# Kernel optimization log

Hardware: AMD Instinct MI355X
Metric: run time of the kernel (lower is better)

The kernel has to match this reference:

```python
import jax, jax.numpy as jnp
import numpy as np

B, S, D_MODEL = 2, 2048, 768
N_QK, D_QK = 16, 16
N_OV, D_OV = 256, 1
VKV = 16
ROT_DIM, ROT_BASE = 16, 10000.0
SCALE = D_QK ** 0.5  # attn_scale defaults to sqrt(d_qk_head)


def _rotary_sin_cos(n_ctx, rotary_dim, base):
    # TransformerLens-style, non-adjacent pairs (GPT-NeoX)
    pos = jnp.arange(n_ctx, dtype=jnp.float32)
    dim = jnp.arange(rotary_dim // 2, dtype=jnp.float32)
    freq = base ** (dim / (rotary_dim / 2))
    freq = jnp.concatenate([freq, freq])  # 'd -> (2 d)'
    angles = pos[:, None] / freq[None, :]  # [n_ctx, rotary_dim]
    return jnp.sin(angles), jnp.cos(angles)


def _apply_rotary(x, sin, cos):
    # x: [B, S, H, d_head]; rotate first ROT_DIM dims, pass through the rest
    s = x.shape[1]
    xr = x[..., :ROT_DIM]
    half = ROT_DIM // 2
    rot = jnp.concatenate([-xr[..., half:], xr[..., :half]], axis=-1)  # rotate_every_two (non-adjacent)
    xr = xr * cos[:s, None, :] + rot * sin[:s, None, :]
    return jnp.concatenate([xr, x[..., ROT_DIM:]], axis=-1) if x.shape[-1] > ROT_DIM else xr


def setup_inputs() -> dict:
    key = jax.random.key(0)
    ks = jax.random.split(key, 6)
    std_qk = np.sqrt(2.0 / (D_MODEL * D_QK))   # kaiming fan_in for [H, d_model, d_head]
    std_v = np.sqrt(2.0 / (D_MODEL * D_OV))
    std_o = np.sqrt(2.0 / (D_OV * D_MODEL))
    std_vk = np.sqrt(2.0 / (N_QK * D_QK))
    return {
        "resid": jax.random.normal(ks[0], (B, S, D_MODEL), jnp.float32),
        "W_Q": jax.random.normal(ks[1], (N_QK, D_MODEL, D_QK), jnp.float32) * std_qk,
        "W_K": jax.random.normal(ks[2], (N_QK, D_MODEL, D_QK), jnp.float32) * std_qk,
        "W_V": jax.random.normal(ks[3], (N_OV, D_MODEL, D_OV), jnp.float32) * std_v,
        "W_O": jax.random.normal(ks[4], (N_OV, D_OV, D_MODEL), jnp.float32) * std_o,
        "b_Q": jnp.zeros((N_QK, D_QK), jnp.float32),
        "b_K": jnp.zeros((N_QK, D_QK), jnp.float32),
        "b_V": jnp.zeros((N_OV, D_OV), jnp.float32),
        "b_O": jnp.zeros((D_MODEL,), jnp.float32),
        "virtual_k": jax.random.normal(ks[5], (VKV, N_QK, D_QK), jnp.float32) * std_vk,
        "virtual_v": jnp.zeros((VKV, N_OV, D_OV), jnp.float32),
    }


def reference(resid, W_Q, W_K, W_V, W_O, b_Q, b_K, b_V, b_O, virtual_k, virtual_v):
    b, s, _ = resid.shape
    sin, cos = _rotary_sin_cos(s, ROT_DIM, ROT_BASE)

    q = jnp.einsum('bsd,hde->bshe', resid, W_Q) + b_Q  # [B,S,N_QK,D_QK]
    k = jnp.einsum('bsd,hde->bshe', resid, W_K) + b_K
    v = jnp.einsum('bsd,hde->bshe', resid, W_V) + b_V  # [B,S,N_OV,1]

    q = _apply_rotary(q, sin, cos)
    k = _apply_rotary(k, sin, cos)

    # append virtual KV along key axis
    k = jnp.concatenate([k, jnp.broadcast_to(virtual_k[None], (b, VKV, N_QK, D_QK))], axis=1)
    v = jnp.concatenate([v, jnp.broadcast_to(virtual_v[None], (b, VKV, N_OV, D_OV))], axis=1)

    scores = jnp.einsum('bqhe,bkhe->bhqk', q, k) / SCALE  # [B,H,S,S+VKV]
    i = jnp.arange(s)[:, None]
    j = jnp.arange(s + VKV)[None, :]
    mask = (j - i) <= VKV  # tril(.., diagonal=VKV)
    scores = jnp.where(mask, scores, -jnp.inf)
    pattern = jax.nn.softmax(scores, axis=-1)
    pattern = jnp.where(jnp.isnan(pattern), 0.0, pattern)

    r = N_OV // N_QK
    v_r = v.transpose(0, 2, 1, 3).reshape(b, N_QK, r, s + VKV, D_OV)  # [B,n_qk,r,K,1]
    z = jnp.einsum('bnqk,bnrkh->bnrqh', pattern, v_r)  # [B,n_qk,r,S,1]
    z = z.reshape(b, N_OV, s, D_OV).transpose(0, 2, 1, 3)  # [B,S,N_OV,1]

    out = jnp.einsum('bqhd,hdm->bqm', z, W_O) + b_O  # [B,S,D_MODEL]
    return out
```

## Files before the change

kernel.cpp:

```cpp
#include <hip/hip_runtime.h>
#include <hip/hip_bf16.h>
#include <math.h>

#define B_   2
#define S_   2048
#define DM   768
#define H_   16
#define C_   256
#define VKV_ 16
#define SK   2064
#define SKP  2080
#define NT_  65

#define TSPLIT 16
#define MAXSP  5
#define NACT   164

typedef __attribute__((ext_vector_type(8))) short short8;
typedef __attribute__((ext_vector_type(4))) short short4v;
typedef __attribute__((ext_vector_type(4))) float f32x4;
typedef __attribute__((ext_vector_type(16))) float f32x16;
typedef __attribute__((ext_vector_type(4))) unsigned uint4v;

#define QSCALE 0.360673760222240851f
#define L2B8   1.6609640474436811f

__device__ __forceinline__ short tobf(float f) {
    union { float f; unsigned u; } x; x.f = f;
    unsigned r = x.u + 0x7FFFu + ((x.u >> 16) & 1u);
    return (short)(r >> 16);
}
__device__ __forceinline__ float frombf_lo(unsigned u) {
    union { unsigned u; float f; } x; x.u = u << 16; return x.f;
}
__device__ __forceinline__ float frombf_hi(unsigned u) {
    union { unsigned u; float f; } x; x.u = u & 0xFFFF0000u; return x.f;
}

__device__ __forceinline__ void gload_lds16(const short* g, short* l) {
    __builtin_amdgcn_global_load_lds(
        (const __attribute__((address_space(1))) unsigned int*)g,
        (__attribute__((address_space(3))) unsigned int*)l, 16, 0, 0);
}

#define NRES (4096*768/4)
#define NWQ  (768*768)
#define NWO  (768*256)
__global__ __launch_bounds__(256) void conv_all(
    const float* __restrict__ resid,
    const float* __restrict__ WQ, const float* __restrict__ WK,
    const float* __restrict__ WV, const float* __restrict__ WO,
    const float* __restrict__ bQ, const float* __restrict__ bK,
    const float* __restrict__ bV,
    const float* __restrict__ vKp, const float* __restrict__ vVp,
    short* __restrict__ Ab, short* __restrict__ Wqkv_t,
    short* __restrict__ WtO, float* __restrict__ bqkv,
    short* __restrict__ Kb2, short* __restrict__ Vt3)
{
    int t = blockIdx.x * 256 + threadIdx.x;
    if (t < NRES) {
        float4 v = *(const float4*)(resid + (size_t)t * 4);
        short4v o = { tobf(v.x), tobf(v.y), tobf(v.z), tobf(v.w) };
        *(short4v*)(Ab + (size_t)t * 4) = o;
        return;
    }
    t -= NRES;
    if (t < NWQ) {
        int cc = t / 768, d = t % 768;
        float w;
        if (cc < 256)      w = WQ[((size_t)(cc >> 4) * DM + d) * 16 + (cc & 15)];
        else if (cc < 512) w = WK[((size_t)((cc - 256) >> 4) * DM + d) * 16 + (cc & 15)];
        else               w = WV[(size_t)(cc - 512) * DM + d];
        Wqkv_t[t] = tobf(w);
        return;
    }
    t -= NWQ;
    if (t < NWO) {
        int c = t & 255, m = t >> 8;
        WtO[t] = tobf(WO[(size_t)c * DM + m]);
        return;
    }
    t -= NWO;
    if (t < 768) {
        bqkv[t] = (t < 256) ? bQ[t] : (t < 512 ? bK[t - 256] : bV[t - 512]);
        return;
    }
    t -= 768;
    if (t < 32 * 32) {
        const int bh = t >> 5;
        const int s  = S_ + (t & 31);
        const int h  = bh & 15;
        short kb[16], vb[16];
        if (s < SK) {
            const int tt = s - S_;
#pragma unroll
            for (int e = 0; e < 16; ++e) {
                kb[e] = tobf(vKp[(size_t)tt * 256 + h * 16 + e]);
                vb[e] = tobf(vVp[(size_t)tt * 256 + h * 16 + e]);
            }
        } else {
#pragma unroll
            for (int e = 0; e < 16; ++e) { kb[e] = 0; vb[e] = 0; }
        }
        const int t5 = s >> 5;
        short* kbase = Kb2 + ((size_t)bh * NT_ + t5) * 512 + (s & 31) * 8;
#pragma unroll
        for (int e = 0; e < 8; ++e)  { kbase[e] = kb[e]; kbase[256 + e] = kb[e + 8]; }
        short* vbase = Vt3 + ((size_t)bh * NT_ + t5) * 1024
                     + ((s >> 4) & 1) * 512 + ((s >> 3) & 1) * 8 + (s & 7);
#pragma unroll
        for (int dv = 0; dv < 16; ++dv) vbase[dv * 16] = vb[dv];
    }
}

__global__ __launch_bounds__(256) void mm_qkv(
    const short* __restrict__ A, const short* __restrict__ Bt,
    const float* __restrict__ bias,
    short* __restrict__ Qb2, short* __restrict__ Kb2, short* __restrict__ Vt3)
{
    __shared__ short As[128 * 64];
    __shared__ short Bs[64 * 64];

    const int tid  = threadIdx.x;
    const int w    = tid >> 6;
    const int lane = tid & 63;
    const int wm   = w >> 1, wn = w & 1;
    const int g    = lane >> 4, c = lane & 15;
    const int m0   = blockIdx.y * 128;
    const int n0   = blockIdx.x * 64;

    f32x4 acc[4][2];
#pragma unroll
    for (int i = 0; i < 4; ++i)
#pragma unroll
        for (int j = 0; j < 2; ++j) acc[i][j] = (f32x4){0.f, 0.f, 0.f, 0.f};

    const int lr = lane >> 3;
    const int lc = lane & 7;

    for (int k0 = 0; k0 < 768; k0 += 64) {
#pragma unroll
        for (int i = 0; i < 4; ++i) {
            const int ch  = i * 4 + w;
            const int row = ch * 8 + lr;
            const int scc = lc ^ (row & 7);
            gload_lds16(A + (size_t)(m0 + row) * 768 + k0 + scc * 8, As + ch * 512);
        }
#pragma unroll
        for (int i = 0; i < 2; ++i) {
            const int ch  = i * 4 + w;
            const int row = ch * 8 + lr;
            const int scc = lc ^ (row & 7);
            gload_lds16(Bt + (size_t)(n0 + row) * 768 + k0 + scc * 8, Bs + ch * 512);
        }
        __syncthreads();
#pragma unroll
        for (int kk = 0; kk < 64; kk += 32) {
            short8 af[4], bf[2];
#pragma unroll
            for (int i = 0; i < 4; ++i) {
                const int row = wm * 64 + i * 16 + c;
                const int sc  = ((kk >> 3) + g) ^ (row & 7);
                af[i] = *(const short8*)(As + row * 64 + sc * 8);
            }
#pragma unroll
            for (int j = 0; j < 2; ++j) {
                const int row = wn * 32 + j * 16 + c;
                const int sc  = ((kk >> 3) + g) ^ (row & 7);
                bf[j] = *(const short8*)(Bs + row * 64 + sc * 8);
            }
#pragma unroll
            for (int i = 0; i < 4; ++i)
#pragma unroll
                for (int j = 0; j < 2; ++j)
                    acc[i][j] = __builtin_amdgcn_mfma_f32_16x16x32_bf16(
                        af[i], bf[j], acc[i][j], 0, 0, 0);
        }
        __syncthreads();
    }

    const float bv0 = bias[n0 + wn * 32 + c];
    const float bv1 = bias[n0 + wn * 32 + 16 + c];

    if (n0 < 512) {
        const int isQ = (n0 < 256) ? 1 : 0;
        const float invf = __builtin_amdgcn_exp2f(-(float)(c & 7) * L2B8);
        const int h0 = (((n0 + wn * 32) & 255) >> 4);
        const int elo = (c & 8) ? 0 : 1;
#pragma unroll
        for (int i = 0; i < 4; ++i) {
#pragma unroll
            for (int r = 0; r < 4; ++r) {
                const int row = m0 + wm * 64 + i * 16 + 4 * g + r;
                const int s   = row & 2047;
                const int b   = row >> 11;
                float sn, cs;
                __sincosf((float)s * invf, &sn, &cs);
#pragma unroll
                for (int j = 0; j < 2; ++j) {
                    float val = acc[i][j][r] + (j ? bv1 : bv0);
                    float par = __shfl_xor(val, 8);
                    float rot = elo ? -par : par;
                    float out = val * cs + rot * sn;
                    if (isQ) out *= QSCALE;
                    const int bh = b * 16 + h0 + j;
                    const size_t base = isQ
                        ? ((size_t)bh * 64 + (s >> 5)) * 512
                        : (size_t)4 * 1024 * 1024 * 0 + ((size_t)bh * NT_ + (s >> 5)) * 512;
                    short* dst = (isQ ? Qb2 : Kb2) + base
                               + (s & 31) * 8 + (c >> 3) * 256 + (c & 7);
                    *dst = tobf(out);
                }
            }
        }
    } else {
        const int h0 = ((n0 + wn * 32 - 512) >> 4);
#pragma unroll
        for (int i = 0; i < 4; ++i) {
#pragma unroll
            for (int r = 0; r < 4; ++r) {
                const int row = m0 + wm * 64 + i * 16 + 4 * g + r;
                const int s   = row & 2047;
                const int b   = row >> 11;
#pragma unroll
                for (int j = 0; j < 2; ++j) {
                    float val = acc[i][j][r] + (j ? bv1 : bv0);
                    const int bh = b * 16 + h0 + j;
                    short* dst = Vt3 + ((size_t)bh * NT_ + (s >> 5)) * 1024
                               + ((s >> 4) & 1) * 512 + ((s >> 3) & 1) * 8 + (s & 7)
                               + c * 16;
                    *dst = tobf(val);
                }
            }
        }
    }
}

__global__ __launch_bounds__(256) void mm_out(
    const short* __restrict__ A, const short* __restrict__ Bt,
    const float* __restrict__ bias, float* __restrict__ Cout)
{
    __shared__ short As[128 * 64];
    __shared__ short Bs[64 * 64];

    const int tid  = threadIdx.x;
    const int w    = tid >> 6;
    const int lane = tid & 63;
    const int wm   = w >> 1, wn = w & 1;
    const int g    = lane >> 4, c = lane & 15;
    const int m0   = blockIdx.y * 128;
    const int n0   = blockIdx.x * 64;

    f32x4 acc[4][2];
#pragma unroll
    for (int i = 0; i < 4; ++i)
#pragma unroll
        for (int j = 0; j < 2; ++j) acc[i][j] = (f32x4){0.f, 0.f, 0.f, 0.f};

    const int lr = lane >> 3;
    const int lc = lane & 7;

    for (int k0 = 0; k0 < 256; k0 += 64) {
#pragma unroll
        for (int i = 0; i < 4; ++i) {
            const int ch  = i * 4 + w;
            const int row = ch * 8 + lr;
            const int scc = lc ^ (row & 7);
            gload_lds16(A + (size_t)(m0 + row) * 256 + k0 + scc * 8, As + ch * 512);
        }
#pragma unroll
        for (int i = 0; i < 2; ++i) {
            const int ch  = i * 4 + w;
            const int row = ch * 8 + lr;
            const int scc = lc ^ (row & 7);
            gload_lds16(Bt + (size_t)(n0 + row) * 256 + k0 + scc * 8, Bs + ch * 512);
        }
        __syncthreads();
#pragma unroll
        for (int kk = 0; kk < 64; kk += 32) {
            short8 af[4], bf[2];
#pragma unroll
            for (int i = 0; i < 4; ++i) {
                const int row = wm * 64 + i * 16 + c;
                const int sc  = ((kk >> 3) + g) ^ (row & 7);
                af[i] = *(const short8*)(As + row * 64 + sc * 8);
            }
#pragma unroll
            for (int j = 0; j < 2; ++j) {
                const int row = wn * 32 + j * 16 + c;
                const int sc  = ((kk >> 3) + g) ^ (row & 7);
                bf[j] = *(const short8*)(Bs + row * 64 + sc * 8);
            }
#pragma unroll
            for (int i = 0; i < 4; ++i)
#pragma unroll
                for (int j = 0; j < 2; ++j)
                    acc[i][j] = __builtin_amdgcn_mfma_f32_16x16x32_bf16(
                        af[i], bf[j], acc[i][j], 0, 0, 0);
        }
        __syncthreads();
    }
#pragma unroll
    for (int i = 0; i < 4; ++i)
#pragma unroll
        for (int j = 0; j < 2; ++j) {
            const int col = n0 + wn * 32 + j * 16 + c;
            const float bv = bias[col];
#pragma unroll
            for (int r = 0; r < 4; ++r) {
                const int row = m0 + wm * 64 + i * 16 + 4 * g + r;
                Cout[(size_t)row * DM + col] = acc[i][j][r] + bv;
            }
        }
}

__global__ __launch_bounds__(256) void attn_split(
    const short* __restrict__ Qb2, const short* __restrict__ Kb2,
    const short* __restrict__ Vt3, unsigned* __restrict__ PartA,
    float* __restrict__ PartL)
{
    const int w    = threadIdx.x >> 6;
    const int lane = threadIdx.x & 63;
    const int wid  = blockIdx.x * 4 + w;
    const int bh   = wid / NACT;
    const int r    = wid - bh * NACT;
    int qt, sp;
    if (r < 49)       { sp = 1; qt = 15 + r; }
    else if (r < 82)  { sp = 2; qt = 31 + (r - 49); }
    else if (r < 99)  { sp = 3; qt = 47 + (r - 82); }
    else if (r == 99) { sp = 4; qt = 63; }
    else              { sp = 0; qt = 163 - r; }

    const int nt   = qt + 2;
    const int t0   = sp * TSPLIT;
    const int tend = min(t0 + TSPLIT, nt);

    const int hi = lane >> 5;
    const int qc = lane & 31;
    const int q0 = qt * 32;

    const f32x16 zero16 = {0,0,0,0,0,0,0,0,0,0,0,0,0,0,0,0};

    short8 qf = *(const short8*)(Qb2 + ((size_t)bh * 64 + qt) * 512 + lane * 8);

    f32x16 acc = zero16;
    float lsum = 0.f;

    const short* kbase = Kb2 + (size_t)bh * NT_ * 512 + lane * 8;
    const short* vbase = Vt3 + (size_t)bh * NT_ * 1024 + (lane & 15) * 16 + hi * 8;
    const int qv16  = q0 + qc + 16;
    const int tmask = (q0 + 17) >> 5;

#define LK(tt)  (*(const short8*)(kbase + (size_t)(tt) * 512))
#define LVA(tt) (*(const short8*)(vbase + (size_t)(tt) * 1024))
#define LVB(tt) (*(const short8*)(vbase + (size_t)(tt) * 1024 + 512))

#define SOFTMAX_TILE(S, tt, B1, B2)                                          \
    {                                                                        \
        if ((tt) >= tmask) {                                                 \
            const int kt_ = (tt) * 32;                                       \
            _Pragma("unroll")                                                \
            for (int rr = 0; rr < 16; ++rr) {                                \
                const int key = kt_ + (rr & 3) + 8 * (rr >> 2) + 4 * hi;     \
                S[rr] = (key <= qv16) ? S[rr] : -INFINITY;                   \
            }                                                                \
        }                                                                    \
        unsigned pk[8];                                                      \
        _Pragma("unroll")                                                    \
        for (int jj = 0; jj < 8; ++jj) {                                     \
            const float p0 = __builtin_amdgcn_exp2f(S[2 * jj]);              \
            const float p1 = __builtin_amdgcn_exp2f(S[2 * jj + 1]);          \
            lsum += p0 + p1;                                                 \
            asm("v_cvt_pk_bf16_f32 %0, %1, %2" : "=v"(pk[jj]) : "v"(p0), "v"(p1)); \
        }                                                                    \
        unsigned a0 = pk[0], a2 = pk[2], a1 = pk[1], a3 = pk[3];             \
        unsigned a4 = pk[4], a6 = pk[6], a5 = pk[5], a7 = pk[7];             \
        asm("v_permlane32_swap_b32 %0, %1" : "+v"(a0), "+v"(a2));            \
        asm("v_permlane32_swap_b32 %0, %1" : "+v"(a1), "+v"(a3));            \
        asm("v_permlane32_swap_b32 %0, %1" : "+v"(a4), "+v"(a6));            \
        asm("v_permlane32_swap_b32 %0, %1" : "+v"(a5), "+v"(a7));            \
        B1.u[0] = a0; B1.u[1] = a1; B1.u[2] = a2; B1.u[3] = a3;              \
        B2.u[0] = a4; B2.u[1] = a5; B2.u[2] = a6; B2.u[3] = a7;              \
    }

    const int npair_end = t0 + ((tend - t0) & ~1);

    if (t0 < npair_end) {
        short8 kfA = LK(t0),     vaA = LVA(t0),     vvA = LVB(t0);
        short8 kfB = LK(t0 + 1), vaB = LVA(t0 + 1), vvB = LVB(t0 + 1);

        for (int t = t0; t < npair_end; t += 2) {
            short8 kfA_n = kfA, vaA_n = vaA, vvA_n = vvA;
            short8 kfB_n = kfB, vaB_n = vaB, vvB_n = vvB;
            if (t + 2 < npair_end) {
                kfA_n = LK(t + 2); vaA_n = LVA(t + 2); vvA_n = LVB(t + 2);
                kfB_n = LK(t + 3); vaB_n = LVA(t + 3); vvB_n = LVB(t + 3);
            }

            f32x16 S0 = __builtin_amdgcn_mfma_f32_32x32x16_bf16(kfA, qf, zero16, 0, 0, 0);
            f32x16 S1 = __builtin_amdgcn_mfma_f32_32x32x16_bf16(kfB, qf, zero16, 0, 0, 0);

            union { unsigned u[4]; short8 v; } b1A, b2A, b1B, b2B;
            SOFTMAX_TILE(S0, t,     b1A, b2A);
            SOFTMAX_TILE(S1, t + 1, b1B, b2B);

            acc = __builtin_amdgcn_mfma_f32_32x32x16_bf16(vaA, b1A.v, acc, 0, 0, 0);
            acc = __builtin_amdgcn_mfma_f32_32x32x16_bf16(vvA, b2A.v, acc, 0, 0, 0);
            acc = __builtin_amdgcn_mfma_f32_32x32x16_bf16(vaB, b1B.v, acc, 0, 0, 0);
            acc = __builtin_amdgcn_mfma_f32_32x32x16_bf16(vvB, b2B.v, acc, 0, 0, 0);

            kfA = kfA_n; vaA = vaA_n; vvA = vvA_n;
            kfB = kfB_n; vaB = vaB_n; vvB = vvB_n;
        }
    }
    if (npair_end < tend) {
        const int t = npair_end;
        short8 kf = LK(t), va = LVA(t), vv = LVB(t);
        f32x16 S0 = __builtin_amdgcn_mfma_f32_32x32x16_bf16(kf, qf, zero16, 0, 0, 0);
        union { unsigned u[4]; short8 v; } b1, b2;
        SOFTMAX_TILE(S0, t, b1, b2);
        acc = __builtin_amdgcn_mfma_f32_32x32x16_bf16(va, b1.v, acc, 0, 0, 0);
        acc = __builtin_amdgcn_mfma_f32_32x32x16_bf16(vv, b2.v, acc, 0, 0, 0);
    }

    uint4v pa;
    asm("v_cvt_pk_bf16_f32 %0, %1, %2" : "=v"(pa.x) : "v"(acc[0]), "v"(acc[1]));
    asm("v_cvt_pk_bf16_f32 %0, %1, %2" : "=v"(pa.y) : "v"(acc[2]), "v"(acc[3]));
    asm("v_cvt_pk_bf16_f32 %0, %1, %2" : "=v"(pa.z) : "v"(acc[4]), "v"(acc[5]));
    asm("v_cvt_pk_bf16_f32 %0, %1, %2" : "=v"(pa.w) : "v"(acc[6]), "v"(acc[7]));

    const int pidx = (bh * 64 + qt) * MAXSP + sp;
    *(uint4v*)(PartA + ((size_t)pidx * 64 + lane) * 4) = pa;

    lsum += __shfl_xor(lsum, 32);
    if (hi == 0) PartL[(size_t)pidx * 32 + qc] = lsum;
}

__global__ __launch_bounds__(256) void attn_combine(
    const unsigned* __restrict__ PartA, const float* __restrict__ PartL,
    short* __restrict__ Zb)
{
    const int w    = threadIdx.x >> 6;
    const int lane = threadIdx.x & 63;
    const int wid  = blockIdx.x * 4 + w;
    const int bh   = wid >> 6;
    const int qt   = wid & 63;
    const int hi   = lane >> 5;
    const int qc   = lane & 31;
    const int ns   = (qt + 2 + TSPLIT - 1) / TSPLIT;

    float a[8];
#pragma unroll
    for (int rr = 0; rr < 8; ++rr) a[rr] = 0.f;
    float lsum = 0.f;

    const int pbase = (bh * 64 + qt) * MAXSP;
    for (int sp = 0; sp < ns; ++sp) {
        uint4v pa = *(const uint4v*)(PartA + ((size_t)(pbase + sp) * 64 + lane) * 4);
        a[0] += frombf_lo(pa.x); a[1] += frombf_hi(pa.x);
        a[2] += frombf_lo(pa.y); a[3] += frombf_hi(pa.y);
        a[4] += frombf_lo(pa.z); a[5] += frombf_hi(pa.z);
        a[6] += frombf_lo(pa.w); a[7] += frombf_hi(pa.w);
        lsum += PartL[(size_t)(pbase + sp) * 32 + qc];
    }
    const float inv = 1.f / lsum;

    const int b = bh >> 4, h = bh & 15;
    const int q0 = qt * 32;
    short* zp = Zb + ((size_t)(b * S_ + q0 + qc)) * C_ + h * 16;
    unsigned o01, o23, o45, o67;
    {
        float a0 = a[0] * inv, a1 = a[1] * inv, a2 = a[2] * inv, a3 = a[3] * inv;
        float a4 = a[4] * inv, a5 = a[5] * inv, a6 = a[6] * inv, a7 = a[7] * inv;
        asm("v_cvt_pk_bf16_f32 %0, %1, %2" : "=v"(o01) : "v"(a0), "v"(a1));
        asm("v_cvt_pk_bf16_f32 %0, %1, %2" : "=v"(o23) : "v"(a2), "v"(a3));
        asm("v_cvt_pk_bf16_f32 %0, %1, %2" : "=v"(o45) : "v"(a4), "v"(a5));
        asm("v_cvt_pk_bf16_f32 %0, %1, %2" : "=v"(o67) : "v"(a6), "v"(a7));
    }
    *(unsigned*)(zp + 4 * hi)         = o01;
    *(unsigned*)(zp + 4 * hi + 2)     = o23;
    *(unsigned*)(zp + 8 + 4 * hi)     = o45;
    *(unsigned*)(zp + 8 + 4 * hi + 2) = o67;
}

extern "C" void kernel_launch(void* const* d_in, const int* in_sizes, int n_in,
                              void* d_out, int out_size, void* d_ws, size_t ws_size,
                              hipStream_t stream)
{
    const float* resid = (const float*)d_in[0];
    const float* WQ = (const float*)d_in[1];
    const float* WK = (const float*)d_in[2];
    const float* WV = (const float*)d_in[3];
    const float* WO = (const float*)d_in[4];
    const float* bQ = (const float*)d_in[5];
    const float* bK = (const float*)d_in[6];
    const float* bV = (const float*)d_in[7];
    const float* bO = (const float*)d_in[8];
    const float* vK = (const float*)d_in[9];
    const float* vV = (const float*)d_in[10];
    float* out = (float*)d_out;
    float* ws  = (float*)d_ws;

    short* Zb   = (short*)ws;
    float* bqkv = ws + 3145728;
    short* Ab   = (short*)(ws + 3145728 + 768);
    short* Wqt  = Ab + 3145728;
    short* WtO  = Wqt + 589824;
    short* Qb2  = WtO + 196608;
    short* Kb2  = Qb2 + 1048576;
    short* Vt3  = Kb2 + 1064960;
    unsigned* PartA = (unsigned*)(Vt3 + 2129920);
    float*    PartL = (float*)(PartA + 2621440);

    const int conv_total = NRES + NWQ + NWO + 768 + 1024;
    conv_all<<<dim3((conv_total + 255) / 256), 256, 0, stream>>>(
        resid, WQ, WK, WV, WO, bQ, bK, bV, vK, vV,
        Ab, Wqt, WtO, bqkv, Kb2, Vt3);
    mm_qkv<<<dim3(12, 32), 256, 0, stream>>>(Ab, Wqt, bqkv, Qb2, Kb2, Vt3);
    attn_split<<<dim3(32 * NACT / 4), 256, 0, stream>>>(Qb2, Kb2, Vt3, PartA, PartL);
    attn_combine<<<dim3(512), 256, 0, stream>>>(PartA, PartL, Zb);
    mm_out<<<dim3(12, 32), 256, 0, stream>>>(Zb, WtO, bO, out);
}
```

Measured before the change: 60.91 us.

## Process two query tiles per wave in attn_split to share K/V loads

```diff
diff --git a/kernel.cpp b/kernel.cpp
--- a/kernel.cpp
+++ b/kernel.cpp
@@ -14,7 +14,6 @@
 
 #define TSPLIT 16
 #define MAXSP  5
-#define NACT   164
 
 typedef __attribute__((ext_vector_type(8))) short short8;
 typedef __attribute__((ext_vector_type(4))) short short4v;
@@ -206,7 +205,7 @@
                     const int bh = b * 16 + h0 + j;
                     const size_t base = isQ
                         ? ((size_t)bh * 64 + (s >> 5)) * 512
-                        : (size_t)4 * 1024 * 1024 * 0 + ((size_t)bh * NT_ + (s >> 5)) * 512;
+                        : ((size_t)bh * NT_ + (s >> 5)) * 512;
                     short* dst = (isQ ? Qb2 : Kb2) + base
                                + (s & 31) * 8 + (c >> 3) * 256 + (c & 7);
                     *dst = tobf(out);
@@ -322,47 +321,46 @@
     const int w    = threadIdx.x >> 6;
     const int lane = threadIdx.x & 63;
     const int wid  = blockIdx.x * 4 + w;
-    const int bh   = wid / NACT;
-    const int r    = wid - bh * NACT;
-    int qt, sp;
-    if (r < 49)       { sp = 1; qt = 15 + r; }
-    else if (r < 82)  { sp = 2; qt = 31 + (r - 49); }
-    else if (r < 99)  { sp = 3; qt = 47 + (r - 82); }
-    else if (r == 99) { sp = 4; qt = 63; }
-    else              { sp = 0; qt = 163 - r; }
-
-    const int nt   = qt + 2;
-    const int t0   = sp * TSPLIT;
-    const int tend = min(t0 + TSPLIT, nt);
+    const int bh   = wid / 160;
+    const int rem  = wid - bh * 160;
+    const int qtp  = rem / 5;
+    const int sp   = rem - qtp * 5;
+
+    const int qt0 = 2 * qtp, qt1 = qt0 + 1;
+    const int nt1 = qt1 + 2;
+    const int t0  = sp * TSPLIT;
+    if (t0 >= nt1) return;
+    const int tend = min(t0 + TSPLIT, nt1);
 
     const int hi = lane >> 5;
     const int qc = lane & 31;
-    const int q0 = qt * 32;
 
     const f32x16 zero16 = {0,0,0,0,0,0,0,0,0,0,0,0,0,0,0,0};
 
-    short8 qf = *(const short8*)(Qb2 + ((size_t)bh * 64 + qt) * 512 + lane * 8);
-
-    f32x16 acc = zero16;
-    float lsum = 0.f;
+    short8 qf0 = *(const short8*)(Qb2 + ((size_t)bh * 64 + qt0) * 512 + lane * 8);
+    short8 qf1 = *(const short8*)(Qb2 + ((size_t)bh * 64 + qt1) * 512 + lane * 8);
+
+    f32x16 acc0 = zero16, acc1 = zero16;
+    float ls0 = 0.f, ls1 = 0.f;
 
     const short* kbase = Kb2 + (size_t)bh * NT_ * 512 + lane * 8;
     const short* vbase = Vt3 + (size_t)bh * NT_ * 1024 + (lane & 15) * 16 + hi * 8;
-    const int qv16  = q0 + qc + 16;
-    const int tmask = (q0 + 17) >> 5;
+    const int qv0 = qt0 * 32 + qc + 16;
+    const int qv1 = qv0 + 32;
+    const int tm0 = qt0, tm1 = qt1;
 
 #define LK(tt)  (*(const short8*)(kbase + (size_t)(tt) * 512))
 #define LVA(tt) (*(const short8*)(vbase + (size_t)(tt) * 1024))
 #define LVB(tt) (*(const short8*)(vbase + (size_t)(tt) * 1024 + 512))
 
-#define SOFTMAX_TILE(S, tt, B1, B2)                                          \
+#define SOFTMAX_TILE(S, tt, QV, TM, LS, B1, B2)                              \
     {                                                                        \
-        if ((tt) >= tmask) {                                                 \
+        if ((tt) >= (TM)) {                                                  \
             const int kt_ = (tt) * 32;                                       \
             _Pragma("unroll")                                                \
             for (int rr = 0; rr < 16; ++rr) {                                \
                 const int key = kt_ + (rr & 3) + 8 * (rr >> 2) + 4 * hi;     \
-                S[rr] = (key <= qv16) ? S[rr] : -INFINITY;                   \
+                S[rr] = (key <= (QV)) ? S[rr] : -INFINITY;                   \
             }                                                                \
         }                                                                    \
         unsigned pk[8];                                                      \
@@ -370,7 +368,7 @@
         for (int jj = 0; jj < 8; ++jj) {                                     \
             const float p0 = __builtin_amdgcn_exp2f(S[2 * jj]);              \
             const float p1 = __builtin_amdgcn_exp2f(S[2 * jj + 1]);          \
-            lsum += p0 + p1;                                                 \
+            LS += p0 + p1;                                                   \
             asm("v_cvt_pk_bf16_f32 %0, %1, %2" : "=v"(pk[jj]) : "v"(p0), "v"(p1)); \
         }                                                                    \
         unsigned a0 = pk[0], a2 = pk[2], a1 = pk[1], a3 = pk[3];             \
@@ -383,57 +381,50 @@
         B2.u[0] = a4; B2.u[1] = a5; B2.u[2] = a6; B2.u[3] = a7;              \
     }
 
-    const int npair_end = t0 + ((tend - t0) & ~1);
-
-    if (t0 < npair_end) {
-        short8 kfA = LK(t0),     vaA = LVA(t0),     vvA = LVB(t0);
-        short8 kfB = LK(t0 + 1), vaB = LVA(t0 + 1), vvB = LVB(t0 + 1);
-
-        for (int t = t0; t < npair_end; t += 2) {
-            short8 kfA_n = kfA, vaA_n = vaA, vvA_n = vvA;
-            short8 kfB_n = kfB, vaB_n = vaB, vvB_n = vvB;
-            if (t + 2 < npair_end) {
-                kfA_n = LK(t + 2); vaA_n = LVA(t + 2); vvA_n = LVB(t + 2);
-                kfB_n = LK(t + 3); vaB_n = LVA(t + 3); vvB_n = LVB(t + 3);
-            }
-
-            f32x16 S0 = __builtin_amdgcn_mfma_f32_32x32x16_bf16(kfA, qf, zero16, 0, 0, 0);
-            f32x16 S1 = __builtin_amdgcn_mfma_f32_32x32x16_bf16(kfB, qf, zero16, 0, 0, 0);
-
-            union { unsigned u[4]; short8 v; } b1A, b2A, b1B, b2B;
-            SOFTMAX_TILE(S0, t,     b1A, b2A);
-            SOFTMAX_TILE(S1, t + 1, b1B, b2B);
-
-            acc = __builtin_amdgcn_mfma_f32_32x32x16_bf16(vaA, b1A.v, acc, 0, 0, 0);
-            acc = __builtin_amdgcn_mfma_f32_32x32x16_bf16(vvA, b2A.v, acc, 0, 0, 0);
-            acc = __builtin_amdgcn_mfma_f32_32x32x16_bf16(vaB, b1B.v, acc, 0, 0, 0);
-            acc = __builtin_amdgcn_mfma_f32_32x32x16_bf16(vvB, b2B.v, acc, 0, 0, 0);
-
-            kfA = kfA_n; vaA = vaA_n; vvA = vvA_n;
-            kfB = kfB_n; vaB = vaB_n; vvB = vvB_n;
-        }
-    }
-    if (npair_end < tend) {
-        const int t = npair_end;
-        short8 kf = LK(t), va = LVA(t), vv = LVB(t);
-        f32x16 S0 = __builtin_amdgcn_mfma_f32_32x32x16_bf16(kf, qf, zero16, 0, 0, 0);
-        union { unsigned u[4]; short8 v; } b1, b2;
-        SOFTMAX_TILE(S0, t, b1, b2);
-        acc = __builtin_amdgcn_mfma_f32_32x32x16_bf16(va, b1.v, acc, 0, 0, 0);
-        acc = __builtin_amdgcn_mfma_f32_32x32x16_bf16(vv, b2.v, acc, 0, 0, 0);
-    }
-
-    uint4v pa;
-    asm("v_cvt_pk_bf16_f32 %0, %1, %2" : "=v"(pa.x) : "v"(acc[0]), "v"(acc[1]));
-    asm("v_cvt_pk_bf16_f32 %0, %1, %2" : "=v"(pa.y) : "v"(acc[2]), "v"(acc[3]));
-    asm("v_cvt_pk_bf16_f32 %0, %1, %2" : "=v"(pa.z) : "v"(acc[4]), "v"(acc[5]));
-    asm("v_cvt_pk_bf16_f32 %0, %1, %2" : "=v"(pa.w) : "v"(acc[6]), "v"(acc[7]));
-
-    const int pidx = (bh * 64 + qt) * MAXSP + sp;
-    *(uint4v*)(PartA + ((size_t)pidx * 64 + lane) * 4) = pa;
-
-    lsum += __shfl_xor(lsum, 32);
-    if (hi == 0) PartL[(size_t)pidx * 32 + qc] = lsum;
+    short8 kf = LK(t0), va = LVA(t0), vv = LVB(t0);
+
+    for (int t = t0; t < tend; ++t) {
+        short8 kf_n = kf, va_n = va, vv_n = vv;
+        if (t + 1 < tend) {
+            kf_n = LK(t + 1); va_n = LVA(t + 1); vv_n = LVB(t + 1);
+        }
+
+        f32x16 S0 = __builtin_amdgcn_mfma_f32_32x32x16_bf16(kf, qf0, zero16, 0, 0, 0);
+        f32x16 S1 = __builtin_amdgcn_mfma_f32_32x32x16_bf16(kf, qf1, zero16, 0, 0, 0);
+
+        union { unsigned u[4]; short8 v; } b1A, b2A, b1B, b2B;
+        SOFTMAX_TILE(S0, t, qv0, tm0, ls0, b1A, b2A);
+        SOFTMAX_TILE(S1, t, qv1, tm1, ls1, b1B, b2B);
+
+        acc0 = __builtin_amdgcn_mfma_f32_32x32x16_bf16(va, b1A.v, acc0, 0, 0, 0);
+        acc0 = __builtin_amdgcn_mfma_f32_32x32x16_bf16(vv, b2A.v, acc0, 0, 0, 0);
+        acc1 = __builtin_amdgcn_mfma_f32_32x32x16_bf16(va, b1B.v, acc1, 0, 0, 0);
+        acc1 = __builtin_amdgcn_mfma_f32_32x32x16_bf16(vv, b2B.v, acc1, 0, 0, 0);
+
+        kf = kf_n; va = va_n; vv = vv_n;
+    }
+
+    uint4v pa0, pa1;
+    asm("v_cvt_pk_bf16_f32 %0, %1, %2" : "=v"(pa0.x) : "v"(acc0[0]), "v"(acc0[1]));
+    asm("v_cvt_pk_bf16_f32 %0, %1, %2" : "=v"(pa0.y) : "v"(acc0[2]), "v"(acc0[3]));
+    asm("v_cvt_pk_bf16_f32 %0, %1, %2" : "=v"(pa0.z) : "v"(acc0[4]), "v"(acc0[5]));
+    asm("v_cvt_pk_bf16_f32 %0, %1, %2" : "=v"(pa0.w) : "v"(acc0[6]), "v"(acc0[7]));
+    asm("v_cvt_pk_bf16_f32 %0, %1, %2" : "=v"(pa1.x) : "v"(acc1[0]), "v"(acc1[1]));
+    asm("v_cvt_pk_bf16_f32 %0, %1, %2" : "=v"(pa1.y) : "v"(acc1[2]), "v"(acc1[3]));
+    asm("v_cvt_pk_bf16_f32 %0, %1, %2" : "=v"(pa1.z) : "v"(acc1[4]), "v"(acc1[5]));
+    asm("v_cvt_pk_bf16_f32 %0, %1, %2" : "=v"(pa1.w) : "v"(acc1[6]), "v"(acc1[7]));
+
+    const int pidx0 = (bh * 64 + qt0) * MAXSP + sp;
+    const int pidx1 = (bh * 64 + qt1) * MAXSP + sp;
+    *(uint4v*)(PartA + ((size_t)pidx0 * 64 + lane) * 4) = pa0;
+    *(uint4v*)(PartA + ((size_t)pidx1 * 64 + lane) * 4) = pa1;
+
+    ls0 += __shfl_xor(ls0, 32);
+    ls1 += __shfl_xor(ls1, 32);
+    if (hi == 0) {
+        PartL[(size_t)pidx0 * 32 + qc] = ls0;
+        PartL[(size_t)pidx1 * 32 + qc] = ls1;
+    }
 }
 
 __global__ __launch_bounds__(256) void attn_combine(
@@ -517,7 +508,7 @@
         resid, WQ, WK, WV, WO, bQ, bK, bV, vK, vV,
         Ab, Wqt, WtO, bqkv, Kb2, Vt3);
     mm_qkv<<<dim3(12, 32), 256, 0, stream>>>(Ab, Wqt, bqkv, Qb2, Kb2, Vt3);
-    attn_split<<<dim3(32 * NACT / 4), 256, 0, stream>>>(Qb2, Kb2, Vt3, PartA, PartL);
+    attn_split<<<dim3(32 * 32 * 5 / 4), 256, 0, stream>>>(Qb2, Kb2, Vt3, PartA, PartL);
     attn_combine<<<dim3(512), 256, 0, stream>>>(PartA, PartL, Zb);
     mm_out<<<dim3(12, 32), 256, 0, stream>>>(Zb, WtO, bO, out);
 }
```

New measurement: 81.86 us. 1.34x slower.
